# Performance work log

Hardware: AMD Instinct MI355X
Metric: run time of the kernel (lower is better)

The kernel has to match this reference:

```python
import jax, jax.numpy as jnp
import numpy as np
import math

B, N, D = 4096, 196, 32
M, H, W, NH = 12, 14, 14, 4
DH = D // NH


def _coords():
    # k_coords: (N,2) grid coords; q_coords: first M points of a (sqrt(M)+1)^2 linspace grid
    yy, xx = np.meshgrid(np.arange(H), np.arange(W), indexing='ij')
    k_coords = np.stack([yy.ravel(), xx.ravel()], axis=-1).astype(np.float32)
    g = int(math.sqrt(M)) + 1  # 4
    cy = np.linspace(0, H - 1, g)
    cx = np.linspace(0, W - 1, g)
    gy, gx = np.meshgrid(cy, cx, indexing='ij')
    grid = np.stack([gy.ravel(), gx.ravel()], axis=-1).astype(np.float32)
    q_coords = grid[:M]
    return jnp.asarray(q_coords), jnp.asarray(k_coords)


def setup_inputs() -> dict:
    key = jax.random.key(0)
    ks = jax.random.split(key, 8)
    q_coords, k_coords = _coords()
    return {
        'T': jax.random.normal(ks[0], (B, N, D), jnp.float32),
        'Q': jax.random.normal(ks[1], (M, D), jnp.float32) * 0.02,
        'Wq': jax.random.normal(ks[2], (D, D), jnp.float32) / math.sqrt(D),
        'Wk': jax.random.normal(ks[3], (D, D), jnp.float32) / math.sqrt(D),
        'Wv': jax.random.normal(ks[4], (D, D), jnp.float32) / math.sqrt(D),
        'Wp': jax.random.normal(ks[5], (D, M * D), jnp.float32) / math.sqrt(M * D),
        'bp': jnp.zeros((D,), jnp.float32),
        'rpb_bias': jax.random.normal(ks[6], (NH, 2 * H - 1, 2 * W - 1), jnp.float32) * 0.02,
        'q_coords': q_coords,
        'k_coords': k_coords,
    }


def reference(T, Q, Wq, Wk, Wv, Wp, bp, rpb_bias, q_coords, k_coords):
    # projections (torch Linear: x @ W^T)
    Qp = Q @ Wq.T                      # (M, D)
    K = T @ Wk.T                       # (B, N, D)
    V = T @ Wv.T                       # (B, N, D)
    Qh = Qp.reshape(M, NH, DH).transpose(1, 0, 2)          # (nh, M, Dh)
    Kh = K.reshape(B, N, NH, DH).transpose(0, 2, 1, 3)     # (B, nh, N, Dh)
    Vh = V.reshape(B, N, NH, DH).transpose(0, 2, 1, 3)     # (B, nh, N, Dh)

    content = jnp.einsum('hmd,bhnd->bhmn', Qh, Kh) / math.sqrt(DH)

    # gathered relative position bias: (nh, M, N)
    dy = q_coords[:, None, 0] - k_coords[None, :, 0]
    dx = q_coords[:, None, 1] - k_coords[None, :, 1]
    idx_y = jnp.clip(jnp.round(dy) + (H - 1), 0, 2 * H - 2).astype(jnp.int32)
    idx_x = jnp.clip(jnp.round(dx) + (W - 1), 0, 2 * W - 2).astype(jnp.int32)
    rpb = rpb_bias[:, idx_y, idx_x]

    logits = content + rpb[None]                            # (B, nh, M, N)
    A = jax.nn.softmax(logits, axis=-1)

    A_avg = A.mean(axis=1)                                  # (B, M, N)
    topk = max(1, int(0.05 * N))                            # 9
    topk_mass = jax.lax.top_k(A_avg, topk)[0].sum(-1)       # (B, M)

    P = jnp.clip(A, 1e-12, None)
    Hn = -(P * jnp.log(P)).sum(-1) / math.log(N)            # (B, nh, M)
    head_energy = (1.0 - Hn).transpose(0, 2, 1)             # (B, M, nh)

    S = jnp.einsum('bhmn,bhnd->bhmd', A, Vh).transpose(0, 2, 1, 3).reshape(B, M, D)
    Z = S.reshape(B, M * D) @ Wp.T + bp                     # (B, D)
    A_maps = A_avg.reshape(B, M, H, W)
    return Z, A_maps, head_energy, S, topk_mass
```

## Files before the change

kernel.cpp:

```cpp
#include <hip/hip_runtime.h>
#include <math.h>


typedef float f32x4 __attribute__((ext_vector_type(4)));
typedef float f32x2 __attribute__((ext_vector_type(2)));
typedef _Float16 h2  __attribute__((ext_vector_type(2)));
typedef _Float16 h4v __attribute__((ext_vector_type(4)));
typedef _Float16 h8  __attribute__((ext_vector_type(8)));
typedef __fp16 fp16x2 __attribute__((ext_vector_type(2)));

__device__ __forceinline__ h2 cvt_pk(float a, float b){
  fp16x2 r = __builtin_amdgcn_cvt_pkrtz(a, b);
  return __builtin_bit_cast(h2, r);
}

__device__ __forceinline__ float dot4(float4 a, float4 b){
  return a.x*b.x + a.y*b.y + a.z*b.z + a.w*b.w;
}

template<int CTRL>
__device__ __forceinline__ int idpp(int x, int id){
  return __builtin_amdgcn_update_dpp(id, x, CTRL, 0xF, 0xF, false);
}
__device__ __forceinline__ int wimax_all(int x){
  const int ID = 0;
  x = max(x, idpp<0x111>(x, ID));
  x = max(x, idpp<0x112>(x, ID));
  x = max(x, idpp<0x114>(x, ID));
  x = max(x, idpp<0x118>(x, ID));
  x = max(x, idpp<0x142>(x, ID));
  x = max(x, idpp<0x143>(x, ID));
  return __builtin_amdgcn_readlane(x, 63);
}

__global__ void prologue_kernel(const float* __restrict__ Q, const float* __restrict__ Wq,
                                const float* __restrict__ Wk, const float* __restrict__ rpb,
                                const float* __restrict__ qc, const float* __restrict__ kc,
                                _Float16* __restrict__ G16, float* __restrict__ rpbc32)
{
  __shared__ float Qp[384];
  const int tid = threadIdx.x;
  const int bid = blockIdx.x;

  if (bid == 0){
    for (int i = tid; i < 384; i += 256){
      int m = i >> 5, d = i & 31;
      float a = 0.f;
      #pragma unroll
      for (int c = 0; c < 32; ++c) a += Q[m*32+c] * Wq[d*32+c];
      Qp[i] = a;
    }
    __syncthreads();
    const float s = 0.35355339059327373f;
    for (int i = tid; i < 1536; i += 256){
      int hm = i >> 5, c = i & 31;
      int hh = hm / 12, mm = hm - 12*hh;
      float a = 0.f;
      #pragma unroll
      for (int dh = 0; dh < 8; ++dh) a += Qp[mm*32 + hh*8 + dh] * Wk[(hh*8+dh)*32 + c];
      G16[i] = (_Float16)(a * s);
    }
  }
  int i = bid*256 + tid;
  if (i < 9984){
    int mh = i / 208, n = i - mh*208;
    float v;
    if (n < 196){
      int hh = mh / 12, mm = mh - 12*hh;
      float dy = qc[2*mm]   - kc[2*n];
      float dx = qc[2*mm+1] - kc[2*n+1];
      int iy = (int)rintf(dy) + 13; iy = iy < 0 ? 0 : (iy > 26 ? 26 : iy);
      int ix = (int)rintf(dx) + 13; ix = ix < 0 ? 0 : (ix > 26 ? 26 : ix);
      v = rpb[hh*729 + iy*27 + ix];
    } else {
      v = -60000.0f;
    }
    rpbc32[i] = v;
  }
}

__device__ __forceinline__ int ttoff(int n, int c8){
  return (n>>2)*128 + ((c8>>1)<<6) + ((n&3)<<4) + ((c8&1)<<3);
}

__global__ __launch_bounds__(256, 5) void fused_main(
    const float* __restrict__ T, const float* __restrict__ Wv, const float* __restrict__ Wp,
    const float* __restrict__ bp, const _Float16* __restrict__ G16,
    const float* __restrict__ rpbc32, float* __restrict__ out)
{
  __shared__ __align__(128) char smem[32544];
  _Float16* TT = (_Float16*)smem;
  _Float16* As = (_Float16*)(smem + 13312);
  float*    U  = (float*)smem;
  float*    Ss = (float*)(smem + 7168);

  const int b    = blockIdx.x;
  const int tid  = threadIdx.x;
  const int lane = tid & 63;
  const int h    = tid >> 6;
  const int r15  = lane & 15;
  const int g    = lane >> 4;

  float* outZ = out;
  float* outA = out + 131072;
  float* outE = out + 9764864;
  float* outS = out + 9961472;
  float* outK = out + 11534336;

  const float* Tb = T + (size_t)b*6272;
  #pragma unroll
  for (int ii = 0; ii < 3; ++ii){
    int i = tid + ii*256;
    int n = i >> 2, c8 = i & 3;
    const f32x4* src = (const f32x4*)(Tb + n*32 + c8*8);
    f32x4 v0 = __builtin_nontemporal_load(src);
    f32x4 v1 = __builtin_nontemporal_load(src + 1);
    h2 p0 = cvt_pk(v0[0], v0[1]);
    h2 p1 = cvt_pk(v0[2], v0[3]);
    h2 p2 = cvt_pk(v1[0], v1[1]);
    h2 p3 = cvt_pk(v1[2], v1[3]);
    h4v lo = __builtin_shufflevector(p0, p1, 0,1,2,3);
    h4v hi = __builtin_shufflevector(p2, p3, 0,1,2,3);
    *(h8*)&TT[ttoff(n, c8)] = __builtin_shufflevector(lo, hi, 0,1,2,3,4,5,6,7);
  }
  if (tid < 64){
    int i = 768 + tid;
    int n = i >> 2, c8 = i & 3;
    h8 hv = {0,0,0,0,0,0,0,0};
    if (n < 196){
      const f32x4* src = (const f32x4*)(Tb + n*32 + c8*8);
      f32x4 v0 = __builtin_nontemporal_load(src);
      f32x4 v1 = __builtin_nontemporal_load(src + 1);
      h2 p0 = cvt_pk(v0[0], v0[1]);
      h2 p1 = cvt_pk(v0[2], v0[3]);
      h2 p2 = cvt_pk(v1[0], v1[1]);
      h2 p3 = cvt_pk(v1[2], v1[3]);
      h4v lo = __builtin_shufflevector(p0, p1, 0,1,2,3);
      h4v hi = __builtin_shufflevector(p2, p3, 0,1,2,3);
      hv = __builtin_shufflevector(lo, hi, 0,1,2,3,4,5,6,7);
    }
    *(h8*)&TT[ttoff(n, c8)] = hv;
  }
  if (tid < 2){
    h8 z = {0,0,0,0,0,0,0,0};
    *(h8*)&As[9600 + tid*8] = z;
  }

  const int mhB = h*12 + (r15 < 12 ? r15 : 11);
  h8 bfrag = *(const h8*)(G16 + mhB*32 + g*8);
  f32x4 acc[13];
  #pragma unroll
  for (int t = 0; t < 13; ++t)
    acc[t] = *(const f32x4*)(rpbc32 + mhB*208 + t*16 + g*4);
  __syncthreads();

  const int rowoff = ((r15>>2)*128) + ((r15&3)<<4) + ((g>>1)<<6) + ((g&1)<<3);
  #pragma unroll
  for (int t = 0; t < 13; ++t){
    h8 af = *(const h8*)&TT[rowoff + t*512];
    acc[t] = __builtin_amdgcn_mfma_f32_16x16x32_f16(af, bfrag, acc[t], 0, 0, 0);
  }

  float mx = -1e30f;
  #pragma unroll
  for (int t = 0; t < 13; ++t)
    mx = fmaxf(mx, fmaxf(fmaxf(acc[t][0], acc[t][1]), fmaxf(acc[t][2], acc[t][3])));
  mx = fmaxf(mx, __shfl_xor(mx, 16));
  mx = fmaxf(mx, __shfl_xor(mx, 32));
  float se = 0.f, te = 0.f;
  #pragma unroll
  for (int t = 0; t < 13; ++t){
    #pragma unroll
    for (int r = 0; r < 4; ++r){
      float d = acc[t][r] - mx;
      float e = __expf(d);
      se += e; te += d*e;
      acc[t][r] = e;
    }
  }
  se += __shfl_xor(se, 16); se += __shfl_xor(se, 32);
  te += __shfl_xor(te, 16); te += __shfl_xor(te, 32);
  const float inv = 1.f / se;
  if (r15 < 12){
    #pragma unroll
    for (int t = 0; t < 13; ++t){
      if (t == 12){
        if (g >= 2) continue;
      }
      h2 w0 = cvt_pk(acc[t][0]*inv, acc[t][1]*inv);
      h2 w1 = cvt_pk(acc[t][2]*inv, acc[t][3]*inv);
      *(h4v*)&As[mhB*200 + t*16 + g*4] = __builtin_shufflevector(w0, w1, 0,1,2,3);
    }
    if (g == 0){
      const float LOGN_INV = 0.18946127f;
      outE[(size_t)b*48 + r15*4 + h] = 1.0f + (te*inv - __logf(se)) * LOGN_INV;
    }
  }
  __syncthreads();

  f32x4 u0 = {0,0,0,0}, u1 = {0,0,0,0};
  if (h < 3){
    const int arow = h*16 + r15;
    unsigned A0 = (unsigned)(size_t)&TT[0] + (unsigned)(g*512 + r15*8);
    #pragma unroll
    for (int ks = 0; ks < 6; ++ks){
      h8 af = *(const h8*)&As[arow*200 + ks*32 + g*8];
      h4v t0, t1, t2, t3;
      asm volatile("ds_read_b64_tr_b16 %0, %1"            : "=v"(t0) : "v"(A0));
      asm volatile("ds_read_b64_tr_b16 %0, %1 offset:256" : "=v"(t1) : "v"(A0));
      asm volatile("ds_read_b64_tr_b16 %0, %1 offset:128" : "=v"(t2) : "v"(A0));
      asm volatile("ds_read_b64_tr_b16 %0, %1 offset:384" : "=v"(t3) : "v"(A0));
      asm volatile("s_waitcnt lgkmcnt(0)" ::: "memory");
      __builtin_amdgcn_sched_barrier(0);
      h8 b0 = __builtin_shufflevector(t0, t1, 0,1,2,3,4,5,6,7);
      h8 b1 = __builtin_shufflevector(t2, t3, 0,1,2,3,4,5,6,7);
      u0 = __builtin_amdgcn_mfma_f32_16x16x32_f16(af, b0, u0, 0, 0, 0);
      u1 = __builtin_amdgcn_mfma_f32_16x16x32_f16(af, b1, u1, 0, 0, 0);
      A0 += 2048;
    }
    h4v afT = *(const h4v*)&As[arow*200 + 192 + g*4];
    unsigned At = (unsigned)(size_t)&TT[0] + (unsigned)(12288 + g*256 + r15*8);
    h4v bt0, bt1;
    asm volatile("ds_read_b64_tr_b16 %0, %1"            : "=v"(bt0) : "v"(At));
    asm volatile("ds_read_b64_tr_b16 %0, %1 offset:128" : "=v"(bt1) : "v"(At));
    asm volatile("s_waitcnt lgkmcnt(0)" ::: "memory");
    __builtin_amdgcn_sched_barrier(0);
    u0 = __builtin_amdgcn_mfma_f32_16x16x16f16(afT, bt0, u0, 0, 0, 0);
    u1 = __builtin_amdgcn_mfma_f32_16x16x16f16(afT, bt1, u1, 0, 0, 0);
  }

  {
    const bool act = (lane < 49);
    const int nb4 = lane * 4;
    int K00=0,K01=0,K02=0,K03=0, K10=0,K11=0,K12=0,K13=0, K20=0,K21=0,K22=0,K23=0;
    float mass0=0.f, mass1=0.f, mass2=0.f;
    const int m0 = h, m1 = h+4, m2 = h+8;

    #pragma unroll
    for (int mi = 0; mi < 3; ++mi){
      int m = (mi==0) ? m0 : ((mi==1) ? m1 : m2);
      if (act){
        h4v s0 = *(const h4v*)&As[(     m)*200 + nb4];
        h4v s1 = *(const h4v*)&As[(12 + m)*200 + nb4];
        h4v s2 = *(const h4v*)&As[(24 + m)*200 + nb4];
        h4v s3 = *(const h4v*)&As[(36 + m)*200 + nb4];
        h4v sh = (s0 + s1) + (s2 + s3);
        float a0 = 0.25f*(float)sh[0], a1 = 0.25f*(float)sh[1];
        float a2 = 0.25f*(float)sh[2], a3 = 0.25f*(float)sh[3];
        float* amrow = outA + (size_t)b*2352 + m*196 + nb4;
        f32x2 o0 = {a0, a1}, o1 = {a2, a3};
        __builtin_nontemporal_store(o0, (f32x2*)amrow);
        __builtin_nontemporal_store(o1, (f32x2*)(amrow + 2));
        int kk0 = (__builtin_bit_cast(int, a0) & ~0xFF) | (lane << 2) | 0;
        int kk1 = (__builtin_bit_cast(int, a1) & ~0xFF) | (lane << 2) | 1;
        int kk2 = (__builtin_bit_cast(int, a2) & ~0xFF) | (lane << 2) | 2;
        int kk3 = (__builtin_bit_cast(int, a3) & ~0xFF) | (lane << 2) | 3;
        if (mi == 0){ K00=kk0; K01=kk1; K02=kk2; K03=kk3; }
        else if (mi == 1){ K10=kk0; K11=kk1; K12=kk2; K13=kk3; }
        else { K20=kk0; K21=kk1; K22=kk2; K23=kk3; }
      }
    }
    #pragma unroll
    for (int k = 0; k < 9; ++k){
      int g0 = wimax_all(max(max(K00,K01), max(K02,K03)));
      int g1 = wimax_all(max(max(K10,K11), max(K12,K13)));
      int g2 = wimax_all(max(max(K20,K21), max(K22,K23)));
      mass0 += __builtin_bit_cast(float, g0 & ~0xFF);
      mass1 += __builtin_bit_cast(float, g1 & ~0xFF);
      mass2 += __builtin_bit_cast(float, g2 & ~0xFF);
      if (lane == ((g0 >> 2) & 63)){
        int q = g0 & 3;
        if (q==0) K00=0; else if (q==1) K01=0; else if (q==2) K02=0; else K03=0;
      }
      if (lane == ((g1 >> 2) & 63)){
        int q = g1 & 3;
        if (q==0) K10=0; else if (q==1) K11=0; else if (q==2) K12=0; else K13=0;
      }
      if (lane == ((g2 >> 2) & 63)){
        int q = g2 & 3;
        if (q==0) K20=0; else if (q==1) K21=0; else if (q==2) K22=0; else K23=0;
      }
    }
    if (lane == 0){
      __builtin_nontemporal_store(mass0, outK + (size_t)b*12 + m0);
      __builtin_nontemporal_store(mass1, outK + (size_t)b*12 + m1);
      __builtin_nontemporal_store(mass2, outK + (size_t)b*12 + m2);
    }
  }
  __syncthreads();

  if (h < 3){
    #pragma unroll
    for (int r = 0; r < 4; ++r){
      U[(h*16 + g*4 + r)*36 + r15]      = u0[r];
      U[(h*16 + g*4 + r)*36 + 16 + r15] = u1[r];
    }
  }
  __syncthreads();

  for (int md = tid; md < 384; md += 256){
    int m = md >> 5, d = md & 31, hh = d >> 3;
    const float4* Urow = (const float4*)(U + (hh*12 + m)*36);
    const float4* Wvr  = (const float4*)(Wv + d*32);
    float a = 0.f;
    #pragma unroll
    for (int q = 0; q < 8; ++q) a += dot4(Urow[q], Wvr[q]);
    Ss[md] = a;
    __builtin_nontemporal_store(a, outS + (size_t)b*384 + md);
  }
  __syncthreads();

  {
    int d = tid >> 3, j4 = tid & 7;
    const float4* Wp4 = (const float4*)(Wp + d*384);
    const float4* Ss4 = (const float4*)Ss;
    float a = 0.f;
    #pragma unroll
    for (int jj = 0; jj < 12; ++jj){
      int j = j4 + jj*8;
      a += dot4(Wp4[j], Ss4[j]);
    }
    a += __shfl_xor(a, 1);
    a += __shfl_xor(a, 2);
    a += __shfl_xor(a, 4);
    if (j4 == 0)
      __builtin_nontemporal_store(bp[d] + a, outZ + (size_t)b*32 + d);
  }
}

extern "C" void kernel_launch(void* const* d_in, const int* in_sizes, int n_in,
                              void* d_out, int out_size, void* d_ws, size_t ws_size,
                              hipStream_t stream)
{
  const float* T    = (const float*)d_in[0];
  const float* Q    = (const float*)d_in[1];
  const float* Wq   = (const float*)d_in[2];
  const float* Wk   = (const float*)d_in[3];
  const float* Wv   = (const float*)d_in[4];
  const float* Wp   = (const float*)d_in[5];
  const float* bp   = (const float*)d_in[6];
  const float* rpb  = (const float*)d_in[7];
  const float* qc   = (const float*)d_in[8];
  const float* kc   = (const float*)d_in[9];
  _Float16* G16  = (_Float16*)d_ws;
  float* rpbc32  = (float*)((char*)d_ws + 4096);
  float* outp = (float*)d_out;

  prologue_kernel<<<40, 256, 0, stream>>>(Q, Wq, Wk, rpb, qc, kc, G16, rpbc32);
  fused_main<<<4096, 256, 0, stream>>>(T, Wv, Wp, bp, G16, rpbc32, outp);
}
```

Baseline: 71.04 us.

## Batch all PV-stage LDS transpose reads before MFMAs and lighten barriers

```diff
diff --git a/kernel.cpp b/kernel.cpp
--- a/kernel.cpp
+++ b/kernel.cpp
@@ -16,6 +16,12 @@
 
 __device__ __forceinline__ float dot4(float4 a, float4 b){
   return a.x*b.x + a.y*b.y + a.z*b.z + a.w*b.w;
+}
+
+__device__ __forceinline__ void barrier_lds(){
+  asm volatile("s_waitcnt lgkmcnt(0)" ::: "memory");
+  __builtin_amdgcn_s_barrier();
+  asm volatile("" ::: "memory");
 }
 
 template<int CTRL>
@@ -83,7 +89,11 @@
   return (n>>2)*128 + ((c8>>1)<<6) + ((n&3)<<4) + ((c8&1)<<3);
 }
 
-__global__ __launch_bounds__(256, 5) void fused_main(
+#define TRRD(dst, base, off) \
+  asm volatile("ds_read_b64_tr_b16 %0, %1 offset:" #off : "=v"(dst) : "v"(base))
+#define SH8(a, b) __builtin_shufflevector(a, b, 0,1,2,3,4,5,6,7)
+
+__global__ __launch_bounds__(256, 4) void fused_main(
     const float* __restrict__ T, const float* __restrict__ Wv, const float* __restrict__ Wp,
     const float* __restrict__ bp, const _Float16* __restrict__ G16,
     const float* __restrict__ rpbc32, float* __restrict__ out)
@@ -152,7 +162,7 @@
   #pragma unroll
   for (int t = 0; t < 13; ++t)
     acc[t] = *(const f32x4*)(rpbc32 + mhB*208 + t*16 + g*4);
-  __syncthreads();
+  barrier_lds();
 
   const int rowoff = ((r15>>2)*128) + ((r15&3)<<4) + ((g>>1)<<6) + ((g&1)<<3);
   #pragma unroll
@@ -196,37 +206,46 @@
       outE[(size_t)b*48 + r15*4 + h] = 1.0f + (te*inv - __logf(se)) * LOGN_INV;
     }
   }
-  __syncthreads();
+  barrier_lds();
 
   f32x4 u0 = {0,0,0,0}, u1 = {0,0,0,0};
   if (h < 3){
     const int arow = h*16 + r15;
+    const _Float16* Ab = &As[arow*200 + g*8];
+    h8 af0 = *(const h8*)(Ab);
+    h8 af1 = *(const h8*)(Ab + 32);
+    h8 af2 = *(const h8*)(Ab + 64);
+    h8 af3 = *(const h8*)(Ab + 96);
+    h8 af4 = *(const h8*)(Ab + 128);
+    h8 af5 = *(const h8*)(Ab + 160);
+    h4v afT = *(const h4v*)&As[arow*200 + 192 + g*4];
     unsigned A0 = (unsigned)(size_t)&TT[0] + (unsigned)(g*512 + r15*8);
-    #pragma unroll
-    for (int ks = 0; ks < 6; ++ks){
-      h8 af = *(const h8*)&As[arow*200 + ks*32 + g*8];
-      h4v t0, t1, t2, t3;
-      asm volatile("ds_read_b64_tr_b16 %0, %1"            : "=v"(t0) : "v"(A0));
-      asm volatile("ds_read_b64_tr_b16 %0, %1 offset:256" : "=v"(t1) : "v"(A0));
-      asm volatile("ds_read_b64_tr_b16 %0, %1 offset:128" : "=v"(t2) : "v"(A0));
-      asm volatile("ds_read_b64_tr_b16 %0, %1 offset:384" : "=v"(t3) : "v"(A0));
-      asm volatile("s_waitcnt lgkmcnt(0)" ::: "memory");
-      __builtin_amdgcn_sched_barrier(0);
-      h8 b0 = __builtin_shufflevector(t0, t1, 0,1,2,3,4,5,6,7);
-      h8 b1 = __builtin_shufflevector(t2, t3, 0,1,2,3,4,5,6,7);
-      u0 = __builtin_amdgcn_mfma_f32_16x16x32_f16(af, b0, u0, 0, 0, 0);
-      u1 = __builtin_amdgcn_mfma_f32_16x16x32_f16(af, b1, u1, 0, 0, 0);
-      A0 += 2048;
-    }
-    h4v afT = *(const h4v*)&As[arow*200 + 192 + g*4];
     unsigned At = (unsigned)(size_t)&TT[0] + (unsigned)(12288 + g*256 + r15*8);
-    h4v bt0, bt1;
-    asm volatile("ds_read_b64_tr_b16 %0, %1"            : "=v"(bt0) : "v"(At));
-    asm volatile("ds_read_b64_tr_b16 %0, %1 offset:128" : "=v"(bt1) : "v"(At));
+    h4v t00,t01,t02,t03, t10,t11,t12,t13, t20,t21,t22,t23,
+        t30,t31,t32,t33, t40,t41,t42,t43, t50,t51,t52,t53, tt0,tt1;
+    TRRD(t00, A0, 0);     TRRD(t01, A0, 256);   TRRD(t02, A0, 128);   TRRD(t03, A0, 384);
+    TRRD(t10, A0, 2048);  TRRD(t11, A0, 2304);  TRRD(t12, A0, 2176);  TRRD(t13, A0, 2432);
+    TRRD(t20, A0, 4096);  TRRD(t21, A0, 4352);  TRRD(t22, A0, 4224);  TRRD(t23, A0, 4480);
+    TRRD(t30, A0, 6144);  TRRD(t31, A0, 6400);  TRRD(t32, A0, 6272);  TRRD(t33, A0, 6528);
+    TRRD(t40, A0, 8192);  TRRD(t41, A0, 8448);  TRRD(t42, A0, 8320);  TRRD(t43, A0, 8576);
+    TRRD(t50, A0, 10240); TRRD(t51, A0, 10496); TRRD(t52, A0, 10368); TRRD(t53, A0, 10624);
+    TRRD(tt0, At, 0);     TRRD(tt1, At, 128);
     asm volatile("s_waitcnt lgkmcnt(0)" ::: "memory");
     __builtin_amdgcn_sched_barrier(0);
-    u0 = __builtin_amdgcn_mfma_f32_16x16x16f16(afT, bt0, u0, 0, 0, 0);
-    u1 = __builtin_amdgcn_mfma_f32_16x16x16f16(afT, bt1, u1, 0, 0, 0);
+    u0 = __builtin_amdgcn_mfma_f32_16x16x32_f16(af0, SH8(t00,t01), u0, 0, 0, 0);
+    u1 = __builtin_amdgcn_mfma_f32_16x16x32_f16(af0, SH8(t02,t03), u1, 0, 0, 0);
+    u0 = __builtin_amdgcn_mfma_f32_16x16x32_f16(af1, SH8(t10,t11), u0, 0, 0, 0);
+    u1 = __builtin_amdgcn_mfma_f32_16x16x32_f16(af1, SH8(t12,t13), u1, 0, 0, 0);
+    u0 = __builtin_amdgcn_mfma_f32_16x16x32_f16(af2, SH8(t20,t21), u0, 0, 0, 0);
+    u1 = __builtin_amdgcn_mfma_f32_16x16x32_f16(af2, SH8(t22,t23), u1, 0, 0, 0);
+    u0 = __builtin_amdgcn_mfma_f32_16x16x32_f16(af3, SH8(t30,t31), u0, 0, 0, 0);
+    u1 = __builtin_amdgcn_mfma_f32_16x16x32_f16(af3, SH8(t32,t33), u1, 0, 0, 0);
+    u0 = __builtin_amdgcn_mfma_f32_16x16x32_f16(af4, SH8(t40,t41), u0, 0, 0, 0);
+    u1 = __builtin_amdgcn_mfma_f32_16x16x32_f16(af4, SH8(t42,t43), u1, 0, 0, 0);
+    u0 = __builtin_amdgcn_mfma_f32_16x16x32_f16(af5, SH8(t50,t51), u0, 0, 0, 0);
+    u1 = __builtin_amdgcn_mfma_f32_16x16x32_f16(af5, SH8(t52,t53), u1, 0, 0, 0);
+    u0 = __builtin_amdgcn_mfma_f32_16x16x16f16(afT, tt0, u0, 0, 0, 0);
+    u1 = __builtin_amdgcn_mfma_f32_16x16x16f16(afT, tt1, u1, 0, 0, 0);
   }
 
   {
@@ -287,7 +306,7 @@
       __builtin_nontemporal_store(mass2, outK + (size_t)b*12 + m2);
     }
   }
-  __syncthreads();
+  barrier_lds();
 
   if (h < 3){
     #pragma unroll
@@ -296,7 +315,7 @@
       U[(h*16 + g*4 + r)*36 + 16 + r15] = u1[r];
     }
   }
-  __syncthreads();
+  barrier_lds();
 
   for (int md = tid; md < 384; md += 256){
     int m = md >> 5, d = md & 31, hh = d >> 3;
@@ -308,7 +327,7 @@
     Ss[md] = a;
     __builtin_nontemporal_store(a, outS + (size_t)b*384 + md);
   }
-  __syncthreads();
+  barrier_lds();
 
   {
     int d = tid >> 3, j4 = tid & 7;
```

New measurement: 70.99 us. Within noise of the previous version (-0.1%).
